# Kernel tuning notes

Measured on AMD Instinct MI355X. Metric: run time of the kernel, lower is better.

Reference implementation:

```python
import jax, jax.numpy as jnp
import numpy as np
from jax import lax

TAU = 2.0        # LIF membrane time constant (init_tau)
VTH = 1.0        # v_threshold
EPS = 1e-5       # BatchNorm eps
ALPHA = 2.0      # ATan surrogate alpha (spikingjelly default)

@jax.custom_vjp
def spike(x):
    # Heaviside forward, ATan surrogate backward
    return (x >= 0.0).astype(x.dtype)

def _spike_fwd(x):
    return spike(x), x

def _spike_bwd(x, g):
    sg = (ALPHA / 2.0) / (1.0 + (jnp.pi / 2.0 * ALPHA * x) ** 2)
    return (g * sg,)

spike.defvjp(_spike_fwd, _spike_bwd)


def setup_inputs() -> dict:
    key = jax.random.key(0)
    k0, k1 = jax.random.split(key, 2)
    B, T, Cin, H = 32, 2048, 80, 256
    x = jax.random.normal(k0, (B, T, Cin), dtype=jnp.float32)
    conv_w = jax.random.normal(k1, (H, Cin, 3), dtype=jnp.float32) * (1.0 / np.sqrt(Cin * 3))
    conv_b = jnp.zeros((H,), dtype=jnp.float32)
    gamma = jnp.ones((H,), dtype=jnp.float32)
    beta = jnp.zeros((H,), dtype=jnp.float32)
    return {"x": x, "conv_w": conv_w, "conv_b": conv_b, "gamma": gamma, "beta": beta}


def reference(x, conv_w, conv_b, gamma, beta):
    # x: (B, T, Cin) -> trans1 -> (B, Cin, T)
    xc = jnp.transpose(x, (0, 2, 1))
    # Conv1d k=3 stride=1 pad=1 -> (B, H, T)
    y = lax.conv_general_dilated(xc, conv_w, window_strides=(1,), padding=[(1, 1)],
                                 dimension_numbers=("NCH", "OIH", "NCH"))
    y = y + conv_b[None, :, None]
    # trans2 -> (T, B, H) multi-step layout
    y = jnp.transpose(y, (2, 0, 1))
    # Multi-step BatchNorm1d over channel H (stats over T and B, training mode)
    mean = y.mean(axis=(0, 1))
    var = y.var(axis=(0, 1))
    y = (y - mean) * lax.rsqrt(var + EPS) * gamma + beta
    # LIF recurrence, decay_input=False, hard reset to 0, detach_reset
    decay = 1.0 - 1.0 / TAU
    v0 = jnp.zeros(y.shape[1:], dtype=y.dtype)  # (B, H)

    def step(v, xt):
        v = v * decay + xt
        s = spike(v - VTH)
        v = v * (1.0 - lax.stop_gradient(s))  # detach_reset=True
        return v, s

    _, s_seq = lax.scan(step, v0, y)
    return s_seq  # (T, B, H) spike train
```

## Files before the change

kernel.cpp:

```cpp
#include <hip/hip_runtime.h>
#include <hip/hip_bf16.h>

#define T_DIM 2048
#define B_DIM 32
#define CIN   80
#define H_DIM 256
#define TT    64
#define NTB   (T_DIM / TT)
#define NBLK  (B_DIM * NTB)
#define KTOT  (CIN * 3)
#define KPAD  256

#define CHUNKS 32
#define CLEN  (T_DIM / CHUNKS)
#define WARM  48
#define SEG   8

#define RCLEN 64
#define RCH   (T_DIM / RCLEN)
#define RNT   (RCLEN + WARM)
#define RNH   16
#define VSTR  (RNT + 1)

#define NPART 64
#define JPER  (NBLK / NPART)

#define DELTA 5e-6

#define XPR 68
#define XPC 88

typedef unsigned short u16;
typedef __attribute__((ext_vector_type(8))) __bf16 bf16x8;
typedef __attribute__((ext_vector_type(4))) float f32x4;

#define PS_OFF  ((size_t)64)
#define PQ_OFF  (PS_OFF + (size_t)NBLK * H_DIM * 8)
#define PAR_OFF (PQ_OFF + (size_t)NBLK * H_DIM * 8)
#define WT_OFF  (PAR_OFF + (size_t)768 * 8)
#define WTF_OFF (WT_OFF + (size_t)H_DIM * KTOT * 8)
#define PA_OFF  (WTF_OFF + (size_t)H_DIM * KTOT * 4)
#define PB_OFF  (PA_OFF + (size_t)NPART * H_DIM * 8)
#define FLG_OFF (PB_OFF + (size_t)NPART * H_DIM * 8)
#define WTB_OFF (FLG_OFF + (size_t)8192)
#define WTB_SZ  ((size_t)3 * H_DIM * KPAD * 2)
#define Y_OFF   (WTB_OFF + WTB_SZ)
#define Y_ELEMS ((size_t)T_DIM * B_DIM * H_DIM)

__device__ __forceinline__ double bf2d(u16 u) {
    union { unsigned int i; float f; } cv;
    cv.i = ((unsigned int)u) << 16;
    return (double)cv.f;
}

__device__ __forceinline__ float bf2f(u16 u) {
    union { unsigned int i; float f; } cv;
    cv.i = ((unsigned int)u) << 16;
    return cv.f;
}

__device__ __forceinline__ double ld_in(const void* p, int i, int isbf) {
    if (isbf) return bf2d(((const u16*)p)[i]);
    return (double)((const float*)p)[i];
}

__device__ __forceinline__ float ldf(const void* p, int i, int isbf) {
    if (isbf) return bf2f(((const u16*)p)[i]);
    return ((const float*)p)[i];
}

__global__ __launch_bounds__(256) void k_prep(const u16* __restrict__ xu,
                                              const void* __restrict__ w,
                                              int* __restrict__ flag,
                                              double* __restrict__ wt,
                                              float* __restrict__ wtf,
                                              __bf16* __restrict__ wtb) {
    __shared__ int cnt[256];
    __shared__ int isbf_s;
    const int tid = threadIdx.x;
    int c = 0;
    for (int j = 0; j < 8; j++) {
        u16 u = xu[tid * 8 + j];
        int e = (u >> 7) & 0xFF;
        if ((u & 0x7FFF) == 0 || (e >= 97 && e <= 157)) c++;
    }
    cnt[tid] = c;
    __syncthreads();
    for (int off = 128; off > 0; off >>= 1) {
        if (tid < off) cnt[tid] += cnt[tid + off];
        __syncthreads();
    }
    if (tid == 0) isbf_s = (cnt[0] >= 1639) ? 1 : 0;
    __syncthreads();
    const int isbf = isbf_s;

    if (blockIdx.x < 240) {
        int idx = blockIdx.x * 256 + tid;
        int h = idx / KTOT;
        int r = idx - h * KTOT;
        int ci = r / 3;
        int dk = r - 3 * ci;
        double v = ld_in(w, idx, isbf);
        wt[(size_t)r * H_DIM + h] = v;
        wtf[(size_t)r * H_DIM + h] = (float)v;
        float vf = (float)v;
        __bf16 h1 = (__bf16)vf; float r1 = vf - (float)h1;
        __bf16 h2 = (__bf16)r1; float r2 = r1 - (float)h2;
        __bf16 h3 = (__bf16)r2;
        const size_t kcol = (size_t)h * KPAD + (dk * 80 + ci);
        wtb[kcol] = h1;
        wtb[(size_t)H_DIM * KPAD + kcol] = h2;
        wtb[(size_t)2 * H_DIM * KPAD + kcol] = h3;
    } else {
        if (tid < 64) {
            const int l = tid, row = l & 15, hi = l >> 4;
            bf16x8 af, bff;
#pragma unroll
            for (int j = 0; j < 8; j++) {
                int k = hi * 8 + j;
                af[j]  = (__bf16)(float)((row * 5 + k * 3) % 7 - 3);
                bff[j] = (__bf16)(float)((k * 11 + row * 2) % 5 - 2);
            }
            f32x4 cc;
#pragma unroll
            for (int r = 0; r < 4; r++) cc[r] = (float)((4 * hi + r) * 100 + row);
            f32x4 d = __builtin_amdgcn_mfma_f32_16x16x32_bf16(af, bff, cc, 0, 0, 0);
            bool ok = true;
#pragma unroll
            for (int r = 0; r < 4; r++) {
                float ref = (float)((4 * hi + r) * 100 + row);
                for (int k = 0; k < 32; k++)
                    ref += (float)(((4 * hi + r) * 5 + k * 3) % 7 - 3) *
                           (float)((k * 11 + row * 2) % 5 - 2);
                if (d[r] != ref) ok = false;
            }
            ok = __all(ok);
            if (l == 0) flag[1] = ok ? 1 : 0;
        }
        if (tid == 0) flag[0] = isbf;
    }
}

__global__ __launch_bounds__(256, 2) void k_convb(const void* __restrict__ x,
                                                  const void* __restrict__ bias,
                                                  const int* __restrict__ flag,
                                                  const __bf16* __restrict__ wtb,
                                                  float* __restrict__ y,
                                                  double* __restrict__ ps,
                                                  double* __restrict__ pq) {
    if (flag[1] != 1) return;
    __shared__ __bf16 xp[3][XPR][XPC];
    const int isbf = flag[0];
    const int tb = blockIdx.x;
    const int b  = blockIdx.y;
    const int t0 = tb * TT;
    const int tid = threadIdx.x;

    for (int idx = tid; idx < 66 * CIN; idx += 256) {
        int tl = idx / CIN;
        int ci = idx - tl * CIN;
        int tg = t0 - 1 + tl;
        float v = 0.0f;
        if (tg >= 0 && tg < T_DIM) v = ldf(x, (b * T_DIM + tg) * CIN + ci, isbf);
        __bf16 h1 = (__bf16)v;  float r1 = v - (float)h1;
        __bf16 h2 = (__bf16)r1; float r2 = r1 - (float)h2;
        __bf16 h3 = (__bf16)r2;
        xp[0][tl][ci] = h1;
        xp[1][tl][ci] = h2;
        xp[2][tl][ci] = h3;
    }
    for (int idx = tid; idx < 2 * XPC; idx += 256) {
        int r = 66 + idx / XPC, cc = idx % XPC;
        xp[0][r][cc] = (__bf16)0.0f; xp[1][r][cc] = (__bf16)0.0f; xp[2][r][cc] = (__bf16)0.0f;
    }
    __syncthreads();

    const int wave = tid >> 6;
    const int lane = tid & 63;
    const int row  = lane & 15;
    const int hi   = lane >> 4;
    const int h0w  = wave * 64;
    const int PL   = XPR * XPC;
    const __bf16* bbase = wtb + (size_t)(h0w + row) * KPAD;
    const size_t BPL = (size_t)H_DIM * KPAD;

    f32x4 acc[4][4];
#pragma unroll
    for (int m = 0; m < 4; m++)
#pragma unroll
        for (int n = 0; n < 4; n++)
#pragma unroll
            for (int r = 0; r < 4; r++) acc[m][n][r] = 0.0f;

    bf16x8 bb[3][3];
#pragma unroll
    for (int g = 0; g < 3; g++) {
        const int kb = (g >> 2) * 32 + hi * 8;
        const __bf16* bp = bbase + (size_t)(g & 3) * 16 * KPAD + kb;
        bb[g][0] = *(const bf16x8*)bp;
        bb[g][1] = *(const bf16x8*)(bp + BPL);
        bb[g][2] = *(const bf16x8*)(bp + 2 * BPL);
    }

    bf16x8 a[2][4][3];
    {
        const int kb0 = hi * 8;
        const int dk = (kb0 >= 160) ? 2 : ((kb0 >= 80) ? 1 : 0);
        const int ci0 = kb0 - dk * 80;
#pragma unroll
        for (int m = 0; m < 4; m++) {
            const __bf16* ap = &xp[0][row + m * 16 + dk][ci0];
            a[0][m][0] = *(const bf16x8*)ap;
            a[0][m][1] = *(const bf16x8*)(ap + PL);
            a[0][m][2] = *(const bf16x8*)(ap + 2 * PL);
        }
    }

#pragma unroll
    for (int g = 0; g < 32; g++) {
        const int ks = g >> 2, nf = g & 3, slot = g % 3, ab = ks & 1;

#pragma unroll
        for (int m = 0; m < 4; m++) {
            acc[m][nf] = __builtin_amdgcn_mfma_f32_16x16x32_bf16(a[ab][m][0], bb[slot][0], acc[m][nf], 0, 0, 0);
            acc[m][nf] = __builtin_amdgcn_mfma_f32_16x16x32_bf16(a[ab][m][0], bb[slot][1], acc[m][nf], 0, 0, 0);
            acc[m][nf] = __builtin_amdgcn_mfma_f32_16x16x32_bf16(a[ab][m][1], bb[slot][0], acc[m][nf], 0, 0, 0);
            acc[m][nf] = __builtin_amdgcn_mfma_f32_16x16x32_bf16(a[ab][m][0], bb[slot][2], acc[m][nf], 0, 0, 0);
            acc[m][nf] = __builtin_amdgcn_mfma_f32_16x16x32_bf16(a[ab][m][1], bb[slot][1], acc[m][nf], 0, 0, 0);
            acc[m][nf] = __builtin_amdgcn_mfma_f32_16x16x32_bf16(a[ab][m][2], bb[slot][0], acc[m][nf], 0, 0, 0);
        }

        if (nf == 2 && ks + 1 < 8) {
            const int kb0 = (ks + 1) * 32 + hi * 8;
            const int dk = (kb0 >= 160) ? 2 : ((kb0 >= 80) ? 1 : 0);
            const int ci0 = kb0 - dk * 80;
            const bool pad = (kb0 >= KTOT);
#pragma unroll
            for (int m = 0; m < 4; m++) {
                const __bf16* ap = pad ? &xp[0][66][0] : &xp[0][row + m * 16 + dk][ci0];
                a[ab ^ 1][m][0] = *(const bf16x8*)ap;
                a[ab ^ 1][m][1] = *(const bf16x8*)(ap + PL);
                a[ab ^ 1][m][2] = *(const bf16x8*)(ap + 2 * PL);
            }
        }

        if (g + 3 < 32) {
            const int g3 = g + 3;
            const int kb = (g3 >> 2) * 32 + hi * 8;
            const __bf16* bp = bbase + (size_t)(g3 & 3) * 16 * KPAD + kb;
            bb[slot][0] = *(const bf16x8*)bp;
            bb[slot][1] = *(const bf16x8*)(bp + BPL);
            bb[slot][2] = *(const bf16x8*)(bp + 2 * BPL);
        }
    }

    const int blk = b * NTB + tb;
#pragma unroll
    for (int nf = 0; nf < 4; nf++) {
        const int h_out = h0w + nf * 16 + row;
        const double bv = ld_in(bias, h_out, isbf);
        double s1 = 0.0, s2 = 0.0;
#pragma unroll
        for (int m = 0; m < 4; m++)
#pragma unroll
            for (int r = 0; r < 4; r++) {
                double v = (double)acc[m][nf][r] + bv;
                y[((size_t)(t0 + m * 16 + 4 * hi + r) * B_DIM + b) * H_DIM + h_out] = (float)v;
                s1 += v;
                s2 = fma(v, v, s2);
            }
        s1 += __shfl_xor(s1, 16); s1 += __shfl_xor(s1, 32);
        s2 += __shfl_xor(s2, 16); s2 += __shfl_xor(s2, 32);
        if (hi == 0) {
            ps[(size_t)blk * H_DIM + h0w + nf * 16 + row] = s1;
            pq[(size_t)blk * H_DIM + h0w + nf * 16 + row] = s2;
        }
    }
}

__global__ __launch_bounds__(256, 8) void k_convf(const void* __restrict__ x,
                                                  const void* __restrict__ bias,
                                                  const int* __restrict__ flag,
                                                  const float* __restrict__ wtf,
                                                  float* __restrict__ y,
                                                  double* __restrict__ ps,
                                                  double* __restrict__ pq) {
    if (flag[1] == 1) return;
    __shared__ __align__(16) float xs[CIN * (TT + 2)];
    const int isbf = flag[0];
    const int tb = blockIdx.x;
    const int b  = blockIdx.y;
    const int t0 = tb * TT;

    for (int idx = threadIdx.x; idx < CIN * (TT + 2); idx += 256) {
        int tl = idx / CIN;
        int ci = idx - tl * CIN;
        int tg = t0 - 1 + tl;
        float v = 0.0f;
        if (tg >= 0 && tg < T_DIM) v = ldf(x, (b * T_DIM + tg) * CIN + ci, isbf);
        xs[ci * (TT + 2) + tl] = v;
    }
    __syncthreads();

    const int h = threadIdx.x;
    float acc[TT];
    const float bv = ldf(bias, h, isbf);
#pragma unroll
    for (int i = 0; i < TT; i++) acc[i] = bv;

    const float* wp = wtf + h;
    float w0 = wp[0], w1 = wp[H_DIM], w2 = wp[2 * H_DIM];
    for (int ci = 0; ci < CIN; ci++) {
        float wn0 = 0.0f, wn1 = 0.0f, wn2 = 0.0f;
        if (ci + 1 < CIN) {
            const float* wq = wtf + (size_t)(ci + 1) * 3 * H_DIM + h;
            wn0 = wq[0]; wn1 = wq[H_DIM]; wn2 = wq[2 * H_DIM];
        }
        const float* xr = xs + ci * (TT + 2);
        float x0 = xr[0], x1 = xr[1];
#pragma unroll
        for (int tt = 0; tt < TT; tt += 2) {
            float2 xp2 = *(const float2*)(xr + tt + 2);
            acc[tt]     = fmaf(w2, xp2.x, fmaf(w1, x1,    fmaf(w0, x0, acc[tt])));
            acc[tt + 1] = fmaf(w2, xp2.y, fmaf(w1, xp2.x, fmaf(w0, x1, acc[tt + 1])));
            x0 = xp2.x; x1 = xp2.y;
        }
        w0 = wn0; w1 = wn1; w2 = wn2;
    }

    const int blk = b * NTB + tb;
    double s1 = 0.0, s2 = 0.0;
#pragma unroll
    for (int tt = 0; tt < TT; tt++) {
        y[((size_t)(t0 + tt) * B_DIM + b) * H_DIM + h] = acc[tt];
        double a = (double)acc[tt];
        s1 += a;
        s2 = fma(a, a, s2);
    }
    ps[(size_t)blk * H_DIM + h] = s1;
    pq[(size_t)blk * H_DIM + h] = s2;
}

__global__ __launch_bounds__(256) void k_statsA(const double* __restrict__ ps,
                                                const double* __restrict__ pq,
                                                double* __restrict__ pa,
                                                double* __restrict__ pb) {
    const int h = threadIdx.x;
    const int k = blockIdx.x;
    double s1 = 0.0, s2 = 0.0;
    const int j0 = k * JPER;
    for (int j = j0; j < j0 + JPER; j++) {
        s1 += ps[(size_t)j * H_DIM + h];
        s2 += pq[(size_t)j * H_DIM + h];
    }
    pa[(size_t)k * H_DIM + h] = s1;
    pb[(size_t)k * H_DIM + h] = s2;
}

__global__ __launch_bounds__(256) void k_statsB(const double* __restrict__ pa,
                                                const double* __restrict__ pb,
                                                const void* __restrict__ gamma,
                                                const void* __restrict__ beta,
                                                const int* __restrict__ flag,
                                                double* __restrict__ par) {
    const int isbf = flag[0];
    const int h = threadIdx.x;
    double s1 = 0.0, s2 = 0.0;
    for (int k = 0; k < NPART; k++) {
        s1 += pa[(size_t)k * H_DIM + h];
        s2 += pb[(size_t)k * H_DIM + h];
    }
    const double N = (double)T_DIM * (double)B_DIM;
    double mean = s1 / N;
    double var  = s2 / N - mean * mean;
    double r    = 1.0 / sqrt(var + 1e-5);
    par[h]       = mean;
    par[256 + h] = r * ld_in(gamma, h, isbf);
    par[512 + h] = ld_in(beta, h, isbf);
}

__global__ __launch_bounds__(256, 8) void k_lif(const float* __restrict__ y,
                                                const double* __restrict__ par,
                                                const int* __restrict__ flag,
                                                unsigned char* __restrict__ flg,
                                                void* __restrict__ out) {
    __shared__ float buf[2][SEG * H_DIM];
    const int isbf = flag[0];
    const int c = blockIdx.x, b = blockIdx.y, h = threadIdx.x;
    const int t_out = c * CLEN;
    int t_begin = t_out - WARM; if (t_begin < 0) t_begin = 0;
    const int t_end = t_out + CLEN;
    const int nseg = (t_end - t_begin) / SEG;

    const double m  = par[h];
    const double A  = par[256 + h];
    const double be = par[512 + h];

    const size_t ST = (size_t)B_DIM * H_DIM;
    const float* yb = y + (size_t)b * H_DIM + h;
    u16*   ob16 = (u16*)out + (size_t)b * H_DIM + h;
    float* ob32 = (float*)out + (size_t)b * H_DIM + h;

    {
        float g[SEG];
#pragma unroll
        for (int k = 0; k < SEG; k++) g[k] = yb[(size_t)(t_begin + k) * ST];
#pragma unroll
        for (int k = 0; k < SEG; k++) buf[0][k * H_DIM + h] = g[k];
    }
    __syncthreads();

    double v = 0.0;
    bool anyf = false;
    for (int s = 0; s < nseg; s++) {
        const int cur = s & 1;
        const bool more = (s + 1 < nseg);
        float g[SEG];
        if (more) {
            const int t1 = t_begin + (s + 1) * SEG;
#pragma unroll
            for (int k = 0; k < SEG; k++) g[k] = yb[(size_t)(t1 + k) * ST];
        }
        double r[SEG];
#pragma unroll
        for (int k = 0; k < SEG; k++) r[k] = (double)buf[cur][k * H_DIM + h];
        const int t0s = t_begin + s * SEG;
#pragma unroll
        for (int k = 0; k < SEG; k++) {
            double val = fma(r[k] - m, A, be);
            v = fma(v, 0.5, val);
            double mg = v - 1.0;
            bool sp = mg >= 0.0;
            anyf |= (fabs(mg) < DELTA);
            const int t = t0s + k;
            if (t >= t_out) {
                size_t oi = (size_t)t * ST;
                if (isbf) ob16[oi] = sp ? (u16)0x3F80 : (u16)0;
                else      ob32[oi] = sp ? 1.0f : 0.0f;
            }
            v = sp ? 0.0 : v;
        }
        if (more) {
#pragma unroll
            for (int k = 0; k < SEG; k++) buf[cur ^ 1][k * H_DIM + h] = g[k];
        }
        __syncthreads();
    }
    if (anyf) flg[(b << 8) | h] = 1;
}

__global__ __launch_bounds__(256) void k_repair(const void* __restrict__ x,
                                                const void* __restrict__ bias,
                                                const double* __restrict__ wt,
                                                const double* __restrict__ par,
                                                const int* __restrict__ flag,
                                                const unsigned char* __restrict__ flg,
                                                void* __restrict__ out) {
    __shared__ int nf_s;
    __shared__ u16 hl[256];
    __shared__ float xs[CIN * (RNT + 2)];
    __shared__ double vs[RNH * VSTR];

    const int b = blockIdx.y;
    const int tid = threadIdx.x;

    if (tid == 0) nf_s = 0;
    __syncthreads();
    if (flg[(b << 8) | tid]) { int p = atomicAdd(&nf_s, 1); hl[p] = (u16)tid; }
    __syncthreads();
    const int nf = nf_s;
    if (nf == 0) return;

    const int isbf = flag[0];
    const int t_out = blockIdx.x * RCLEN;
    const int t_begin = t_out - WARM;

    for (int idx = tid; idx < CIN * (RNT + 2); idx += 256) {
        int tl = idx / CIN;
        int ci = idx - tl * CIN;
        int tg = t_begin - 1 + tl;
        float v = 0.0f;
        if (tg >= 0 && tg < T_DIM) v = ldf(x, (b * T_DIM + tg) * CIN + ci, isbf);
        xs[ci * (RNT + 2) + tl] = v;
    }

    const int hi = tid >> 4;
    const int ti = tid & 15;

    for (int g0 = 0; g0 < nf; g0 += RNH) {
        const int h = (g0 + hi < nf) ? (int)hl[g0 + hi] : -1;
        __syncthreads();

        if (h >= 0) {
            const double bv = ld_in(bias, h, isbf);
            const double m  = par[h];
            const double A  = par[256 + h];
            const double be = par[512 + h];
            double acc[7];
#pragma unroll
            for (int k = 0; k < 7; k++) acc[k] = bv;
            const double* wq = wt + h;
            for (int ci = 0; ci < CIN; ci++) {
                const double w0 = wq[0], w1 = wq[H_DIM], w2 = wq[2 * H_DIM];
                wq += 3 * H_DIM;
                const float* xr = xs + ci * (RNT + 2) + ti * 7;
                float xv[9];
#pragma unroll
                for (int j = 0; j < 9; j++) xv[j] = xr[j];
#pragma unroll
                for (int k = 0; k < 7; k++)
                    acc[k] = fma(w0, (double)xv[k],
                             fma(w1, (double)xv[k + 1],
                             fma(w2, (double)xv[k + 2], acc[k])));
            }
#pragma unroll
            for (int k = 0; k < 7; k++) {
                const int tt = ti * 7 + k;
                vs[hi * VSTR + tt] = (t_begin + tt < 0) ? 0.0 : fma(acc[k] - m, A, be);
            }
        }
        __syncthreads();

        if (tid < RNH && g0 + tid < nf) {
            const int h2 = (int)hl[g0 + tid];
            const double* vr = vs + tid * VSTR;
            double v = 0.0;
            for (int tt = 0; tt < RNT; tt++) {
                v = fma(v, 0.5, vr[tt]);
                bool sp = (v - 1.0) >= 0.0;
                const int t = t_begin + tt;
                if (t >= t_out) {
                    size_t oi = ((size_t)t * B_DIM + b) * H_DIM + h2;
                    if (isbf) ((u16*)out)[oi] = sp ? (u16)0x3F80 : (u16)0;
                    else      ((float*)out)[oi] = sp ? 1.0f : 0.0f;
                }
                v = sp ? 0.0 : v;
            }
        }
    }
}

__global__ void k_code(u16* out, float code) {
    if (threadIdx.x == 0 && blockIdx.x == 0) {
        union { unsigned int i; float f; } cv; cv.f = code;
        out[0] = (u16)(cv.i >> 16);
    }
}

extern "C" void kernel_launch(void* const* d_in, const int* in_sizes, int n_in,
                              void* d_out, int out_size, void* d_ws, size_t ws_size,
                              hipStream_t stream) {
    const void* x     = d_in[0];
    const void* w     = d_in[1];
    const void* cb    = d_in[2];
    const void* gamma = d_in[3];
    const void* beta  = d_in[4];

    char* wsb   = (char*)d_ws;
    int* flag   = (int*)wsb;
    double* PS  = (double*)(wsb + PS_OFF);
    double* PQ  = (double*)(wsb + PQ_OFF);
    double* PAR = (double*)(wsb + PAR_OFF);
    double* WT  = (double*)(wsb + WT_OFF);
    float*  WTF = (float*)(wsb + WTF_OFF);
    double* PA  = (double*)(wsb + PA_OFF);
    double* PB  = (double*)(wsb + PB_OFF);
    unsigned char* FLG = (unsigned char*)(wsb + FLG_OFF);
    __bf16* WTB = (__bf16*)(wsb + WTB_OFF);
    float* Yp   = (float*)(wsb + Y_OFF);

    const size_t need = Y_OFF + Y_ELEMS * 4;

    if (ws_size < need) {
        hipMemsetAsync(d_out, 0, (size_t)out_size * 2, stream);
        k_code<<<1, 64, 0, stream>>>((u16*)d_out, 1000.0f);
        return;
    }

    hipMemsetAsync(FLG, 0, 8192 + WTB_SZ, stream);
    k_prep<<<dim3(241), dim3(256), 0, stream>>>((const u16*)x, w, flag, WT, WTF, WTB);
    k_convb<<<dim3(NTB, B_DIM), dim3(256), 0, stream>>>(
        x, cb, flag, WTB, Yp, PS, PQ);
    k_convf<<<dim3(NTB, B_DIM), dim3(256), 0, stream>>>(
        x, cb, flag, WTF, Yp, PS, PQ);
    k_statsA<<<dim3(NPART), dim3(256), 0, stream>>>(PS, PQ, PA, PB);
    k_statsB<<<dim3(1), dim3(256), 0, stream>>>(PA, PB, gamma, beta, flag, PAR);
    k_lif<<<dim3(CHUNKS, B_DIM), dim3(256), 0, stream>>>(Yp, PAR, flag, FLG, d_out);
    k_repair<<<dim3(RCH, B_DIM), dim3(256), 0, stream>>>(
        x, cb, WT, PAR, flag, FLG, d_out);
}
```

Measured before the change: 234.3 us.

## Vectorize conv input staging, deepen B-fragment prefetch, drop LDS buffering in LIF

The conv kernel now loads input pairs with 2-wide vector loads and writes packed bf16x2 values into shared memory, halving the staging loop trips. The B-operand register prefetch ring grows from 3 to 4 slots, so each slot maps to one n-fragment and loads are issued one group further ahead. The LIF kernel drops its shared-memory double buffer and __syncthreads, ping-ponging between two register arrays instead. This removes LDS traffic and barriers at the cost of more registers, and the LIF launch-bounds occupancy hint is removed.

```diff
diff --git a/kernel.cpp b/kernel.cpp
--- a/kernel.cpp
+++ b/kernel.cpp
@@ -32,6 +32,7 @@
 
 typedef unsigned short u16;
 typedef __attribute__((ext_vector_type(8))) __bf16 bf16x8;
+typedef __attribute__((ext_vector_type(2))) __bf16 bf16x2;
 typedef __attribute__((ext_vector_type(4))) float f32x4;
 
 #define PS_OFF  ((size_t)64)
@@ -156,22 +157,38 @@
     const int t0 = tb * TT;
     const int tid = threadIdx.x;
 
-    for (int idx = tid; idx < 66 * CIN; idx += 256) {
-        int tl = idx / CIN;
-        int ci = idx - tl * CIN;
+    for (int idx = tid; idx < 66 * (CIN / 2); idx += 256) {
+        int tl = idx / (CIN / 2);
+        int cp = idx - tl * (CIN / 2);
+        int ci = cp * 2;
         int tg = t0 - 1 + tl;
-        float v = 0.0f;
-        if (tg >= 0 && tg < T_DIM) v = ldf(x, (b * T_DIM + tg) * CIN + ci, isbf);
-        __bf16 h1 = (__bf16)v;  float r1 = v - (float)h1;
-        __bf16 h2 = (__bf16)r1; float r2 = r1 - (float)h2;
-        __bf16 h3 = (__bf16)r2;
-        xp[0][tl][ci] = h1;
-        xp[1][tl][ci] = h2;
-        xp[2][tl][ci] = h3;
-    }
-    for (int idx = tid; idx < 2 * XPC; idx += 256) {
-        int r = 66 + idx / XPC, cc = idx % XPC;
-        xp[0][r][cc] = (__bf16)0.0f; xp[1][r][cc] = (__bf16)0.0f; xp[2][r][cc] = (__bf16)0.0f;
+        float v0 = 0.0f, v1 = 0.0f;
+        if (tg >= 0 && tg < T_DIM) {
+            const size_t base = (size_t)(b * T_DIM + tg) * CIN + ci;
+            if (isbf) {
+                unsigned int u = *(const unsigned int*)((const u16*)x + base);
+                v0 = bf2f((u16)u); v1 = bf2f((u16)(u >> 16));
+            } else {
+                float2 f = *(const float2*)((const float*)x + base);
+                v0 = f.x; v1 = f.y;
+            }
+        }
+        __bf16 a1 = (__bf16)v0; float r1 = v0 - (float)a1;
+        __bf16 a2 = (__bf16)r1; float r2 = r1 - (float)a2;
+        __bf16 a3 = (__bf16)r2;
+        __bf16 c1 = (__bf16)v1; float s1 = v1 - (float)c1;
+        __bf16 c2 = (__bf16)s1; float s2 = s1 - (float)c2;
+        __bf16 c3 = (__bf16)s2;
+        *(bf16x2*)&xp[0][tl][ci] = bf16x2{a1, c1};
+        *(bf16x2*)&xp[1][tl][ci] = bf16x2{a2, c2};
+        *(bf16x2*)&xp[2][tl][ci] = bf16x2{a3, c3};
+    }
+    for (int idx = tid; idx < 2 * (XPC / 2); idx += 256) {
+        int r = 66 + idx / (XPC / 2), cc = (idx % (XPC / 2)) * 2;
+        bf16x2 z = {(__bf16)0.0f, (__bf16)0.0f};
+        *(bf16x2*)&xp[0][r][cc] = z;
+        *(bf16x2*)&xp[1][r][cc] = z;
+        *(bf16x2*)&xp[2][r][cc] = z;
     }
     __syncthreads();
 
@@ -192,10 +209,10 @@
 #pragma unroll
             for (int r = 0; r < 4; r++) acc[m][n][r] = 0.0f;
 
-    bf16x8 bb[3][3];
-#pragma unroll
-    for (int g = 0; g < 3; g++) {
-        const int kb = (g >> 2) * 32 + hi * 8;
+    bf16x8 bb[4][3];
+#pragma unroll
+    for (int g = 0; g < 4; g++) {
+        const int kb = hi * 8;
         const __bf16* bp = bbase + (size_t)(g & 3) * 16 * KPAD + kb;
         bb[g][0] = *(const bf16x8*)bp;
         bb[g][1] = *(const bf16x8*)(bp + BPL);
@@ -218,7 +235,7 @@
 
 #pragma unroll
     for (int g = 0; g < 32; g++) {
-        const int ks = g >> 2, nf = g & 3, slot = g % 3, ab = ks & 1;
+        const int ks = g >> 2, nf = g & 3, slot = g & 3, ab = ks & 1;
 
 #pragma unroll
         for (int m = 0; m < 4; m++) {
@@ -244,10 +261,10 @@
             }
         }
 
-        if (g + 3 < 32) {
-            const int g3 = g + 3;
-            const int kb = (g3 >> 2) * 32 + hi * 8;
-            const __bf16* bp = bbase + (size_t)(g3 & 3) * 16 * KPAD + kb;
+        if (g + 4 < 32) {
+            const int g4 = g + 4;
+            const int kb = (g4 >> 2) * 32 + hi * 8;
+            const __bf16* bp = bbase + (size_t)(g4 & 3) * 16 * KPAD + kb;
             bb[slot][0] = *(const bf16x8*)bp;
             bb[slot][1] = *(const bf16x8*)(bp + BPL);
             bb[slot][2] = *(const bf16x8*)(bp + 2 * BPL);
@@ -379,18 +396,16 @@
     par[512 + h] = ld_in(beta, h, isbf);
 }
 
-__global__ __launch_bounds__(256, 8) void k_lif(const float* __restrict__ y,
-                                                const double* __restrict__ par,
-                                                const int* __restrict__ flag,
-                                                unsigned char* __restrict__ flg,
-                                                void* __restrict__ out) {
-    __shared__ float buf[2][SEG * H_DIM];
+__global__ __launch_bounds__(256) void k_lif(const float* __restrict__ y,
+                                             const double* __restrict__ par,
+                                             const int* __restrict__ flag,
+                                             unsigned char* __restrict__ flg,
+                                             void* __restrict__ out) {
     const int isbf = flag[0];
     const int c = blockIdx.x, b = blockIdx.y, h = threadIdx.x;
     const int t_out = c * CLEN;
     int t_begin = t_out - WARM; if (t_begin < 0) t_begin = 0;
-    const int t_end = t_out + CLEN;
-    const int nseg = (t_end - t_begin) / SEG;
+    const int nseg = (t_out + CLEN - t_begin) / SEG;
 
     const double m  = par[h];
     const double A  = par[256 + h];
@@ -401,51 +416,49 @@
     u16*   ob16 = (u16*)out + (size_t)b * H_DIM + h;
     float* ob32 = (float*)out + (size_t)b * H_DIM + h;
 
-    {
-        float g[SEG];
-#pragma unroll
-        for (int k = 0; k < SEG; k++) g[k] = yb[(size_t)(t_begin + k) * ST];
-#pragma unroll
-        for (int k = 0; k < SEG; k++) buf[0][k * H_DIM + h] = g[k];
-    }
-    __syncthreads();
+    float ga[SEG], gb[SEG];
+#pragma unroll
+    for (int k = 0; k < SEG; k++) ga[k] = yb[(size_t)(t_begin + k) * ST];
 
     double v = 0.0;
     bool anyf = false;
-    for (int s = 0; s < nseg; s++) {
-        const int cur = s & 1;
-        const bool more = (s + 1 < nseg);
-        float g[SEG];
-        if (more) {
-            const int t1 = t_begin + (s + 1) * SEG;
-#pragma unroll
-            for (int k = 0; k < SEG; k++) g[k] = yb[(size_t)(t1 + k) * ST];
-        }
-        double r[SEG];
-#pragma unroll
-        for (int k = 0; k < SEG; k++) r[k] = (double)buf[cur][k * H_DIM + h];
-        const int t0s = t_begin + s * SEG;
-#pragma unroll
-        for (int k = 0; k < SEG; k++) {
-            double val = fma(r[k] - m, A, be);
-            v = fma(v, 0.5, val);
-            double mg = v - 1.0;
-            bool sp = mg >= 0.0;
-            anyf |= (fabs(mg) < DELTA);
-            const int t = t0s + k;
-            if (t >= t_out) {
-                size_t oi = (size_t)t * ST;
-                if (isbf) ob16[oi] = sp ? (u16)0x3F80 : (u16)0;
-                else      ob32[oi] = sp ? 1.0f : 0.0f;
-            }
-            v = sp ? 0.0 : v;
-        }
-        if (more) {
-#pragma unroll
-            for (int k = 0; k < SEG; k++) buf[cur ^ 1][k * H_DIM + h] = g[k];
-        }
-        __syncthreads();
-    }
+
+#define LIF_SEG(GR, TBASE)                                                    \
+    {                                                                         \
+        const int t0s = (TBASE);                                              \
+        _Pragma("unroll")                                                     \
+        for (int k = 0; k < SEG; k++) {                                       \
+            double val = fma((double)GR[k] - m, A, be);                       \
+            v = fma(v, 0.5, val);                                             \
+            double mg = v - 1.0;                                              \
+            bool sp = mg >= 0.0;                                              \
+            anyf |= (fabs(mg) < DELTA);                                       \
+            const int t = t0s + k;                                            \
+            if (t >= t_out) {                                                 \
+                size_t oi = (size_t)t * ST;                                   \
+                if (isbf) ob16[oi] = sp ? (u16)0x3F80 : (u16)0;               \
+                else      ob32[oi] = sp ? 1.0f : 0.0f;                        \
+            }                                                                 \
+            v = sp ? 0.0 : v;                                                 \
+        }                                                                     \
+    }
+
+    for (int s = 0; s < nseg; s += 2) {
+        const int t1 = t_begin + (s + 1) * SEG;
+        if (s + 1 < nseg) {
+#pragma unroll
+            for (int k = 0; k < SEG; k++) gb[k] = yb[(size_t)(t1 + k) * ST];
+        }
+        LIF_SEG(ga, t_begin + s * SEG);
+        const int t2 = t_begin + (s + 2) * SEG;
+        if (s + 2 < nseg) {
+#pragma unroll
+            for (int k = 0; k < SEG; k++) ga[k] = yb[(size_t)(t2 + k) * ST];
+        }
+        if (s + 1 < nseg) LIF_SEG(gb, t1);
+    }
+#undef LIF_SEG
+
     if (anyf) flg[(b << 8) | h] = 1;
 }
 
```

Result: no change. 230.4 us (-1.7%).
